# Performance work log

Hardware: AMD Instinct MI355X
Metric: run time of the kernel (lower is better)

## Reference

```python
import jax, jax.numpy as jnp
import numpy as np

ALPHA = 0.5
N_NODES = 100000
N_EDGES = 1600000
D_IN = 128
D_OUT = 128


def setup_inputs() -> dict:
    key = jax.random.key(0)
    k1, k2, k3, k4, k5, k6 = jax.random.split(key, 6)
    x = jax.random.normal(k1, (N_NODES, D_IN), dtype=jnp.float32)
    edge_index = jax.random.randint(k2, (2, N_EDGES), 0, N_NODES, dtype=jnp.int64)
    # torch Linear default init: U(-1/sqrt(fan_in), 1/sqrt(fan_in)); scale similar here
    s = 1.0 / np.sqrt(D_IN)
    W_src = jax.random.uniform(k3, (D_OUT, D_IN), jnp.float32, -s, s)
    b_src = jax.random.uniform(k4, (D_OUT,), jnp.float32, -s, s)
    W_dst = jax.random.uniform(k5, (D_OUT, D_IN), jnp.float32, -s, s)
    b_dst = jax.random.uniform(k6, (D_OUT,), jnp.float32, -s, s)
    return {"x": x, "edge_index": edge_index, "W_src": W_src, "b_src": b_src,
            "W_dst": W_dst, "b_dst": b_dst}


def _inv_sqrt(deg):
    # deg^{-1/2} with inf -> 0 (isolated nodes)
    return jnp.where(deg > 0, jax.lax.rsqrt(jnp.maximum(deg, 1e-30)), 0.0)


def reference(x, edge_index, W_src, b_src, W_dst, b_dst):
    n = x.shape[0]
    row, col = edge_index[0], edge_index[1]
    ones = jnp.ones(row.shape[0], dtype=x.dtype)
    # degrees of directed adjacency A[row, col] = 1
    deg_out = jax.ops.segment_sum(ones, row, num_segments=n)  # row sums
    deg_in = jax.ops.segment_sum(ones, col, num_segments=n)   # col sums
    # D_out^{-1/2} A D_in^{-1/2} edge weights; transpose norm yields the SAME weights
    w = _inv_sqrt(deg_out)[row] * _inv_sqrt(deg_in)[col]      # [E]
    # adj_norm @ x : aggregate sources (col) into destinations (row)
    agg_fwd = jax.ops.segment_sum(w[:, None] * x[col], row, num_segments=n)  # [N, D_IN]
    # adj_t_norm @ x : aggregate destinations (row) into sources (col)
    agg_bwd = jax.ops.segment_sum(w[:, None] * x[row], col, num_segments=n)  # [N, D_IN]
    out = ALPHA * (agg_fwd @ W_src.T + b_src) + (1.0 - ALPHA) * (agg_bwd @ W_dst.T + b_dst)
    return out
```

## Files before the change

kernel.cpp:

```cpp
#include <hip/hip_runtime.h>
#include <stdint.h>

#define D 128
#define CC 4096
#define CE 2048

typedef __attribute__((ext_vector_type(8))) __bf16 bf16x8;
typedef __attribute__((ext_vector_type(4))) float floatx4;

union FragU { uint4 u; bf16x8 b; };

__device__ __forceinline__ float bf16_lo(uint32_t u) { return __uint_as_float(u << 16); }
__device__ __forceinline__ float bf16_hi(uint32_t u) { return __uint_as_float(u & 0xffff0000u); }
__device__ __forceinline__ uint16_t f32_to_bf16(float f) {
    uint32_t u = __float_as_uint(f);
    uint32_t r = u + 0x7fffu + ((u >> 16) & 1u);
    return (uint16_t)(r >> 16);
}
__device__ __forceinline__ uint32_t pack2(float a, float b) {
    return (uint32_t)f32_to_bf16(a) | ((uint32_t)f32_to_bf16(b) << 16);
}

__global__ __launch_bounds__(256) void k_prep_w(
    const float* __restrict__ Wsrc, const float* __restrict__ bsrc,
    const float* __restrict__ Wdst, const float* __restrict__ bdst,
    uint16_t* __restrict__ WcatT, float* __restrict__ bias)
{
    int t = blockIdx.x * 256 + threadIdx.x;
    if (t < 16384) {
        WcatT[t] = f32_to_bf16(0.5f * Wsrc[t]);
        if (t < 128) bias[t] = 0.5f * (bsrc[t] + bdst[t]);
    } else {
        WcatT[t] = f32_to_bf16(0.5f * Wdst[t - 16384]);
    }
}

__global__ __launch_bounds__(256) void k_count(
    const int* __restrict__ ei, int E, int nbuk, uint32_t* __restrict__ gcount)
{
    __shared__ uint32_t cnt[1024];
    int nb2 = 2 * nbuk;
    for (int j = threadIdx.x; j < nb2; j += 256) cnt[j] = 0;
    __syncthreads();
    int base = blockIdx.x * CC;
    int lim = min(CC, E - base);
    for (int i = threadIdx.x; i < lim; i += 256) {
        int r = ei[base + i];
        int c = ei[E + base + i];
        atomicAdd(&cnt[r >> 8], 1u);
        atomicAdd(&cnt[nbuk + (c >> 8)], 1u);
    }
    __syncthreads();
    for (int j = threadIdx.x; j < nb2; j += 256) {
        uint32_t v = cnt[j];
        if (v) atomicAdd(&gcount[j], v);
    }
}

__global__ __launch_bounds__(256) void k_bases(
    const uint32_t* __restrict__ gcount, uint32_t* __restrict__ pbase,
    uint32_t* __restrict__ gcursor, int nb2)
{
    __shared__ uint32_t s[256];
    uint32_t v[4]; uint32_t tsum = 0;
    int b0 = threadIdx.x * 4;
    #pragma unroll
    for (int j = 0; j < 4; ++j) { v[j] = (b0 + j < nb2) ? gcount[b0 + j] : 0u; tsum += v[j]; }
    s[threadIdx.x] = tsum;
    __syncthreads();
    for (int off = 1; off < 256; off <<= 1) {
        uint32_t t = (threadIdx.x >= (unsigned)off) ? s[threadIdx.x - off] : 0u;
        __syncthreads();
        s[threadIdx.x] += t;
        __syncthreads();
    }
    uint32_t run = s[threadIdx.x] - tsum;
    #pragma unroll
    for (int j = 0; j < 4; ++j) {
        if (b0 + j < nb2) { pbase[b0 + j] = run; gcursor[b0 + j] = run; }
        run += v[j];
    }
}

__global__ __launch_bounds__(256) void k_part(
    const int* __restrict__ ei, int E, int nbuk,
    uint32_t* __restrict__ gcursor, uint32_t* __restrict__ gpairs)
{
    __shared__ uint32_t cnt[1024];
    __shared__ uint32_t loff[1024];
    __shared__ uint32_t gbase[1024];
    __shared__ uint32_t spair[2 * CE];
    __shared__ uint16_t sbid[2 * CE];
    __shared__ uint32_t ssum[256];
    int nb2 = 2 * nbuk;
    for (int j = threadIdx.x; j < nb2; j += 256) cnt[j] = 0;
    __syncthreads();
    int base = blockIdx.x * CE;
    int lim = min(CE, E - base);
    for (int i = threadIdx.x; i < lim; i += 256) {
        int r = ei[base + i];
        int c = ei[E + base + i];
        atomicAdd(&cnt[r >> 8], 1u);
        atomicAdd(&cnt[nbuk + (c >> 8)], 1u);
    }
    __syncthreads();
    uint32_t v0 = 0, v1 = 0, v2 = 0, v3 = 0;
    int b0 = threadIdx.x * 4;
    if (b0 < nb2)     v0 = cnt[b0];
    if (b0 + 1 < nb2) v1 = cnt[b0 + 1];
    if (b0 + 2 < nb2) v2 = cnt[b0 + 2];
    if (b0 + 3 < nb2) v3 = cnt[b0 + 3];
    uint32_t tsum = v0 + v1 + v2 + v3;
    ssum[threadIdx.x] = tsum;
    __syncthreads();
    for (int off = 1; off < 256; off <<= 1) {
        uint32_t t = (threadIdx.x >= (unsigned)off) ? ssum[threadIdx.x - off] : 0u;
        __syncthreads();
        ssum[threadIdx.x] += t;
        __syncthreads();
    }
    uint32_t run = ssum[threadIdx.x] - tsum;
    if (b0 < nb2)     loff[b0]     = run;
    if (b0 + 1 < nb2) loff[b0 + 1] = run + v0;
    if (b0 + 2 < nb2) loff[b0 + 2] = run + v0 + v1;
    if (b0 + 3 < nb2) loff[b0 + 3] = run + v0 + v1 + v2;
    __syncthreads();
    for (int j = threadIdx.x; j < nb2; j += 256) {
        uint32_t c2 = cnt[j];
        gbase[j] = c2 ? atomicAdd(&gcursor[j], c2) : 0u;
        cnt[j] = loff[j];
    }
    __syncthreads();
    for (int i = threadIdx.x; i < lim; i += 256) {
        int r = ei[base + i];
        int c = ei[E + base + i];
        int bf = r >> 8;
        uint32_t sf = atomicAdd(&cnt[bf], 1u);
        spair[sf] = ((uint32_t)c << 8) | (uint32_t)(r & 255);
        sbid[sf] = (uint16_t)bf;
        int bb = nbuk + (c >> 8);
        uint32_t sb = atomicAdd(&cnt[bb], 1u);
        spair[sb] = ((uint32_t)r << 8) | (uint32_t)(c & 255);
        sbid[sb] = (uint16_t)bb;
    }
    __syncthreads();
    int total = 2 * lim;
    for (int s2 = threadIdx.x; s2 < total; s2 += 256) {
        int b = sbid[s2];
        gpairs[gbase[b] + ((uint32_t)s2 - loff[b])] = spair[s2];
    }
}

__global__ __launch_bounds__(256) void k_build(
    const uint32_t* __restrict__ gpairs, const uint32_t* __restrict__ pbase,
    const uint32_t* __restrict__ gcount, int nbuk, int N,
    int* __restrict__ edata, uint32_t* __restrict__ ptrg, uint32_t* __restrict__ degg,
    float* __restrict__ inv_o, float* __restrict__ inv_i)
{
    __shared__ uint32_t hist[256], cur[256], ssum[256];
    int b = blockIdx.x;
    int dir = (b >= nbuk) ? 1 : 0;
    int node0 = (b - dir * nbuk) << 8;
    uint32_t base = pbase[b];
    uint32_t cnt_b = gcount[b];
    hist[threadIdx.x] = 0;
    __syncthreads();
    for (uint32_t i = threadIdx.x; i < cnt_b; i += 256)
        atomicAdd(&hist[gpairs[base + i] & 255u], 1u);
    __syncthreads();
    uint32_t h = hist[threadIdx.x];
    ssum[threadIdx.x] = h;
    __syncthreads();
    for (int off = 1; off < 256; off <<= 1) {
        uint32_t t = (threadIdx.x >= (unsigned)off) ? ssum[threadIdx.x - off] : 0u;
        __syncthreads();
        ssum[threadIdx.x] += t;
        __syncthreads();
    }
    uint32_t excl = ssum[threadIdx.x] - h;
    cur[threadIdx.x] = excl;
    int n = node0 + threadIdx.x;
    if (n < N) {
        ptrg[dir * N + n] = base + excl;
        degg[dir * N + n] = h;
        float iv = h ? rsqrtf((float)h) : 0.0f;
        if (dir == 0) inv_o[n] = iv; else inv_i[n] = iv;
    }
    __syncthreads();
    for (uint32_t i = threadIdx.x; i < cnt_b; i += 256) {
        uint32_t e = gpairs[base + i];
        uint32_t pos = atomicAdd(&cur[e & 255u], 1u);
        edata[base + pos] = (int)(e >> 8);
    }
}

__global__ __launch_bounds__(256, 2) void k_mm(
    const float* __restrict__ x, const uint4* __restrict__ Wt4,
    const float* __restrict__ inv_o, const float* __restrict__ inv_i,
    uint16_t* __restrict__ u2b, uint16_t* __restrict__ v2b, int N)
{
    const int lane = threadIdx.x & 63;
    const int m16 = lane & 15;
    const int quad = lane >> 4;
    const int mat = blockIdx.x & 1;
    uint16_t* outb = mat ? v2b : u2b;
    const float* inv = mat ? inv_o : inv_i;

    bf16x8 Bf[8][4];
    #pragma unroll
    for (int ct = 0; ct < 8; ++ct) {
        #pragma unroll
        for (int ks = 0; ks < 4; ++ks) {
            int n = mat * 128 + ct * 16 + m16;
            FragU f; f.u = Wt4[n * 16 + ks * 4 + quad];
            Bf[ct][ks] = f.b;
        }
    }

    const int ntiles = (N + 15) >> 4;
    const int wslot = (blockIdx.x >> 1) * 4 + (threadIdx.x >> 6);
    const int nslot = (gridDim.x >> 1) * 4;

    for (int t = wslot; t < ntiles; t += nslot) {
        int rowA = t * 16 + m16;
        if (rowA >= N) rowA = N - 1;
        const float4* xr = (const float4*)(x + (long)rowA * 128);
        bf16x8 Af[4];
        #pragma unroll
        for (int ks = 0; ks < 4; ++ks) {
            float4 p0 = xr[ks * 8 + quad * 2];
            float4 p1 = xr[ks * 8 + quad * 2 + 1];
            FragU f;
            f.u.x = pack2(p0.x, p0.y);
            f.u.y = pack2(p0.z, p0.w);
            f.u.z = pack2(p1.x, p1.y);
            f.u.w = pack2(p1.z, p1.w);
            Af[ks] = f.b;
        }
        float iv[4];
        #pragma unroll
        for (int r = 0; r < 4; ++r) {
            int row = t * 16 + quad * 4 + r;
            iv[r] = inv[row < N ? row : 0];
        }
        #pragma unroll
        for (int ct = 0; ct < 8; ++ct) {
            floatx4 acc = {};
            #pragma unroll
            for (int ks = 0; ks < 4; ++ks)
                acc = __builtin_amdgcn_mfma_f32_16x16x32_bf16(Af[ks], Bf[ct][ks], acc, 0, 0, 0);
            #pragma unroll
            for (int r = 0; r < 4; ++r) {
                int row = t * 16 + quad * 4 + r;
                if (row < N)
                    outb[(long)row * 128 + ct * 16 + m16] = f32_to_bf16(acc[r] * iv[r]);
            }
        }
    }
}

__global__ __launch_bounds__(256) void k_gather(
    const uint32_t* __restrict__ u2, const uint32_t* __restrict__ v2,
    const int* __restrict__ edata,
    const uint32_t* __restrict__ ptrg, const uint32_t* __restrict__ degg,
    const float* __restrict__ inv_out, const float* __restrict__ inv_in,
    const float2* __restrict__ bias2, float2* __restrict__ out2, int N)
{
    int lane = threadIdx.x & 63;
    int node = blockIdx.x * 4 + (threadIdx.x >> 6);
    if (node >= N) return;

    uint32_t s0 = ptrg[node],     d0 = degg[node];
    uint32_t s1 = ptrg[N + node], d1 = degg[N + node];

    float fx = 0, fy = 0, bx = 0, by = 0;
    uint32_t k = 0;
    for (; k + 4 <= d0; k += 4) {
        int c0 = edata[s0 + k], c1 = edata[s0 + k + 1];
        int c2 = edata[s0 + k + 2], c3 = edata[s0 + k + 3];
        uint32_t p0 = u2[(long)c0 * 64 + lane];
        uint32_t p1 = u2[(long)c1 * 64 + lane];
        uint32_t p2 = u2[(long)c2 * 64 + lane];
        uint32_t p3 = u2[(long)c3 * 64 + lane];
        fx += bf16_lo(p0) + bf16_lo(p1) + bf16_lo(p2) + bf16_lo(p3);
        fy += bf16_hi(p0) + bf16_hi(p1) + bf16_hi(p2) + bf16_hi(p3);
    }
    for (; k < d0; ++k) {
        uint32_t p = u2[(long)edata[s0 + k] * 64 + lane];
        fx += bf16_lo(p); fy += bf16_hi(p);
    }
    k = 0;
    for (; k + 4 <= d1; k += 4) {
        int c0 = edata[s1 + k], c1 = edata[s1 + k + 1];
        int c2 = edata[s1 + k + 2], c3 = edata[s1 + k + 3];
        uint32_t p0 = v2[(long)c0 * 64 + lane];
        uint32_t p1 = v2[(long)c1 * 64 + lane];
        uint32_t p2 = v2[(long)c2 * 64 + lane];
        uint32_t p3 = v2[(long)c3 * 64 + lane];
        bx += bf16_lo(p0) + bf16_lo(p1) + bf16_lo(p2) + bf16_lo(p3);
        by += bf16_hi(p0) + bf16_hi(p1) + bf16_hi(p2) + bf16_hi(p3);
    }
    for (; k < d1; ++k) {
        uint32_t p = v2[(long)edata[s1 + k] * 64 + lane];
        bx += bf16_lo(p); by += bf16_hi(p);
    }

    float io = inv_out[node], ii = inv_in[node];
    float2 b = bias2[lane];
    out2[(long)node * 64 + lane] =
        make_float2(io * fx + ii * bx + b.x, io * fy + ii * by + b.y);
}

extern "C" void kernel_launch(void* const* d_in, const int* in_sizes, int n_in,
                              void* d_out, int out_size, void* d_ws, size_t ws_size,
                              hipStream_t stream) {
    const int N = in_sizes[0] / D;
    const int E = in_sizes[1] / 2;
    const int nbuk = (N + 255) >> 8;
    const int nb2 = 2 * nbuk;

    const float* x    = (const float*)d_in[0];
    const int*   ei   = (const int*)d_in[1];
    const float* Wsrc = (const float*)d_in[2];
    const float* bsrc = (const float*)d_in[3];
    const float* Wdst = (const float*)d_in[4];
    const float* bdst = (const float*)d_in[5];

    char* ws = (char*)d_ws;
    size_t off = 0;
    uint32_t* gcount = (uint32_t*)(ws + off); off += 1024 * 4;
    uint32_t* pbase  = (uint32_t*)(ws + off); off += 1024 * 4;
    uint32_t* gcur   = (uint32_t*)(ws + off); off += 1024 * 4;
    float*    inv_o  = (float*)(ws + off);    off += (size_t)N * 4;
    float*    inv_i  = (float*)(ws + off);    off += (size_t)N * 4;
    float*    biasc  = (float*)(ws + off);    off += 128 * 4;
    uint16_t* WcatT  = (uint16_t*)(ws + off); off += (size_t)256 * 128 * 2;
    uint32_t* ptrg   = (uint32_t*)(ws + off); off += (size_t)2 * N * 4;
    uint32_t* degg   = (uint32_t*)(ws + off); off += (size_t)2 * N * 4;
    uint32_t* gpairs = (uint32_t*)(ws + off); off += (size_t)2 * E * 4;
    int*      edata  = (int*)(ws + off);      off += (size_t)2 * E * 4;
    uint32_t* u2     = (uint32_t*)(ws + off); off += (size_t)N * 64 * 4;
    uint32_t* v2     = (uint32_t*)(ws + off); off += (size_t)N * 64 * 4;

    hipMemsetAsync(gcount, 0, 1024 * 4, stream);

    k_prep_w<<<128, 256, 0, stream>>>(Wsrc, bsrc, Wdst, bdst, WcatT, biasc);
    k_count<<<(E + CC - 1) / CC, 256, 0, stream>>>(ei, E, nbuk, gcount);
    k_bases<<<1, 256, 0, stream>>>(gcount, pbase, gcur, nb2);
    k_part<<<(E + CE - 1) / CE, 256, 0, stream>>>(ei, E, nbuk, gcur, gpairs);
    k_build<<<nb2, 256, 0, stream>>>(gpairs, pbase, gcount, nbuk, N,
                                     edata, ptrg, degg, inv_o, inv_i);

    k_mm<<<1024, 256, 0, stream>>>(x, (const uint4*)WcatT, inv_o, inv_i,
                                   (uint16_t*)u2, (uint16_t*)v2, N);

    k_gather<<<(N + 3) / 4, 256, 0, stream>>>(u2, v2, edata, ptrg, degg,
                                              inv_o, inv_i, (const float2*)biasc,
                                              (float2*)d_out, N);
}
```

Measured before the change: 358.9 us.

## Fold weight prep into matmul, enlarge edge chunks, unroll gather by eight

Removes the separate weight-conversion kernel: k_mm now reads the fp32 weights directly and converts them to bf16 with the 0.5 scale, and the gather kernel computes the combined bias inline. Chunk sizes for the count and partition kernels are doubled, which means fewer blocks. The gather inner loops are unrolled to eight outstanding loads instead of four. Together these cut one launch and raise memory-level parallelism, at the cost of redundant weight conversion in every matmul block and more register pressure in the gather.

Measured after the change: 365.5 us. About the same (+1.8%).

```diff
diff --git a/kernel.cpp b/kernel.cpp
--- a/kernel.cpp
+++ b/kernel.cpp
@@ -2,8 +2,8 @@
 #include <stdint.h>
 
 #define D 128
-#define CC 4096
-#define CE 2048
+#define CC 8192
+#define CE 4096
 
 typedef __attribute__((ext_vector_type(8))) __bf16 bf16x8;
 typedef __attribute__((ext_vector_type(4))) float floatx4;
@@ -19,20 +19,6 @@
 }
 __device__ __forceinline__ uint32_t pack2(float a, float b) {
     return (uint32_t)f32_to_bf16(a) | ((uint32_t)f32_to_bf16(b) << 16);
-}
-
-__global__ __launch_bounds__(256) void k_prep_w(
-    const float* __restrict__ Wsrc, const float* __restrict__ bsrc,
-    const float* __restrict__ Wdst, const float* __restrict__ bdst,
-    uint16_t* __restrict__ WcatT, float* __restrict__ bias)
-{
-    int t = blockIdx.x * 256 + threadIdx.x;
-    if (t < 16384) {
-        WcatT[t] = f32_to_bf16(0.5f * Wsrc[t]);
-        if (t < 128) bias[t] = 0.5f * (bsrc[t] + bdst[t]);
-    } else {
-        WcatT[t] = f32_to_bf16(0.5f * Wdst[t - 16384]);
-    }
 }
 
 __global__ __launch_bounds__(256) void k_count(
@@ -195,7 +181,8 @@
 }
 
 __global__ __launch_bounds__(256, 2) void k_mm(
-    const float* __restrict__ x, const uint4* __restrict__ Wt4,
+    const float* __restrict__ x,
+    const float* __restrict__ Wsrc, const float* __restrict__ Wdst,
     const float* __restrict__ inv_o, const float* __restrict__ inv_i,
     uint16_t* __restrict__ u2b, uint16_t* __restrict__ v2b, int N)
 {
@@ -205,14 +192,20 @@
     const int mat = blockIdx.x & 1;
     uint16_t* outb = mat ? v2b : u2b;
     const float* inv = mat ? inv_o : inv_i;
+    const float* Wm = mat ? Wdst : Wsrc;
 
     bf16x8 Bf[8][4];
     #pragma unroll
     for (int ct = 0; ct < 8; ++ct) {
         #pragma unroll
         for (int ks = 0; ks < 4; ++ks) {
-            int n = mat * 128 + ct * 16 + m16;
-            FragU f; f.u = Wt4[n * 16 + ks * 4 + quad];
+            const float4* wr = (const float4*)(Wm + (ct * 16 + m16) * 128 + ks * 32 + quad * 8);
+            float4 w0 = wr[0], w1 = wr[1];
+            FragU f;
+            f.u.x = pack2(0.5f * w0.x, 0.5f * w0.y);
+            f.u.y = pack2(0.5f * w0.z, 0.5f * w0.w);
+            f.u.z = pack2(0.5f * w1.x, 0.5f * w1.y);
+            f.u.w = pack2(0.5f * w1.z, 0.5f * w1.w);
             Bf[ct][ks] = f.b;
         }
     }
@@ -264,7 +257,8 @@
     const int* __restrict__ edata,
     const uint32_t* __restrict__ ptrg, const uint32_t* __restrict__ degg,
     const float* __restrict__ inv_out, const float* __restrict__ inv_in,
-    const float2* __restrict__ bias2, float2* __restrict__ out2, int N)
+    const float* __restrict__ bsrc, const float* __restrict__ bdst,
+    float2* __restrict__ out2, int N)
 {
     int lane = threadIdx.x & 63;
     int node = blockIdx.x * 4 + (threadIdx.x >> 6);
@@ -275,30 +269,38 @@
 
     float fx = 0, fy = 0, bx = 0, by = 0;
     uint32_t k = 0;
-    for (; k + 4 <= d0; k += 4) {
-        int c0 = edata[s0 + k], c1 = edata[s0 + k + 1];
-        int c2 = edata[s0 + k + 2], c3 = edata[s0 + k + 3];
-        uint32_t p0 = u2[(long)c0 * 64 + lane];
-        uint32_t p1 = u2[(long)c1 * 64 + lane];
-        uint32_t p2 = u2[(long)c2 * 64 + lane];
-        uint32_t p3 = u2[(long)c3 * 64 + lane];
-        fx += bf16_lo(p0) + bf16_lo(p1) + bf16_lo(p2) + bf16_lo(p3);
-        fy += bf16_hi(p0) + bf16_hi(p1) + bf16_hi(p2) + bf16_hi(p3);
+    for (; k + 8 <= d0; k += 8) {
+        uint32_t p0 = u2[(long)edata[s0 + k]     * 64 + lane];
+        uint32_t p1 = u2[(long)edata[s0 + k + 1] * 64 + lane];
+        uint32_t p2 = u2[(long)edata[s0 + k + 2] * 64 + lane];
+        uint32_t p3 = u2[(long)edata[s0 + k + 3] * 64 + lane];
+        uint32_t p4 = u2[(long)edata[s0 + k + 4] * 64 + lane];
+        uint32_t p5 = u2[(long)edata[s0 + k + 5] * 64 + lane];
+        uint32_t p6 = u2[(long)edata[s0 + k + 6] * 64 + lane];
+        uint32_t p7 = u2[(long)edata[s0 + k + 7] * 64 + lane];
+        fx += bf16_lo(p0) + bf16_lo(p1) + bf16_lo(p2) + bf16_lo(p3)
+            + bf16_lo(p4) + bf16_lo(p5) + bf16_lo(p6) + bf16_lo(p7);
+        fy += bf16_hi(p0) + bf16_hi(p1) + bf16_hi(p2) + bf16_hi(p3)
+            + bf16_hi(p4) + bf16_hi(p5) + bf16_hi(p6) + bf16_hi(p7);
     }
     for (; k < d0; ++k) {
         uint32_t p = u2[(long)edata[s0 + k] * 64 + lane];
         fx += bf16_lo(p); fy += bf16_hi(p);
     }
     k = 0;
-    for (; k + 4 <= d1; k += 4) {
-        int c0 = edata[s1 + k], c1 = edata[s1 + k + 1];
-        int c2 = edata[s1 + k + 2], c3 = edata[s1 + k + 3];
-        uint32_t p0 = v2[(long)c0 * 64 + lane];
-        uint32_t p1 = v2[(long)c1 * 64 + lane];
-        uint32_t p2 = v2[(long)c2 * 64 + lane];
-        uint32_t p3 = v2[(long)c3 * 64 + lane];
-        bx += bf16_lo(p0) + bf16_lo(p1) + bf16_lo(p2) + bf16_lo(p3);
-        by += bf16_hi(p0) + bf16_hi(p1) + bf16_hi(p2) + bf16_hi(p3);
+    for (; k + 8 <= d1; k += 8) {
+        uint32_t p0 = v2[(long)edata[s1 + k]     * 64 + lane];
+        uint32_t p1 = v2[(long)edata[s1 + k + 1] * 64 + lane];
+        uint32_t p2 = v2[(long)edata[s1 + k + 2] * 64 + lane];
+        uint32_t p3 = v2[(long)edata[s1 + k + 3] * 64 + lane];
+        uint32_t p4 = v2[(long)edata[s1 + k + 4] * 64 + lane];
+        uint32_t p5 = v2[(long)edata[s1 + k + 5] * 64 + lane];
+        uint32_t p6 = v2[(long)edata[s1 + k + 6] * 64 + lane];
+        uint32_t p7 = v2[(long)edata[s1 + k + 7] * 64 + lane];
+        bx += bf16_lo(p0) + bf16_lo(p1) + bf16_lo(p2) + bf16_lo(p3)
+            + bf16_lo(p4) + bf16_lo(p5) + bf16_lo(p6) + bf16_lo(p7);
+        by += bf16_hi(p0) + bf16_hi(p1) + bf16_hi(p2) + bf16_hi(p3)
+            + bf16_hi(p4) + bf16_hi(p5) + bf16_hi(p6) + bf16_hi(p7);
     }
     for (; k < d1; ++k) {
         uint32_t p = v2[(long)edata[s1 + k] * 64 + lane];
@@ -306,9 +308,10 @@
     }
 
     float io = inv_out[node], ii = inv_in[node];
-    float2 b = bias2[lane];
+    float b0 = 0.5f * (bsrc[2 * lane]     + bdst[2 * lane]);
+    float b1 = 0.5f * (bsrc[2 * lane + 1] + bdst[2 * lane + 1]);
     out2[(long)node * 64 + lane] =
-        make_float2(io * fx + ii * bx + b.x, io * fy + ii * by + b.y);
+        make_float2(io * fx + ii * bx + b0, io * fy + ii * by + b1);
 }
 
 extern "C" void kernel_launch(void* const* d_in, const int* in_sizes, int n_in,
@@ -333,8 +336,6 @@
     uint32_t* gcur   = (uint32_t*)(ws + off); off += 1024 * 4;
     float*    inv_o  = (float*)(ws + off);    off += (size_t)N * 4;
     float*    inv_i  = (float*)(ws + off);    off += (size_t)N * 4;
-    float*    biasc  = (float*)(ws + off);    off += 128 * 4;
-    uint16_t* WcatT  = (uint16_t*)(ws + off); off += (size_t)256 * 128 * 2;
     uint32_t* ptrg   = (uint32_t*)(ws + off); off += (size_t)2 * N * 4;
     uint32_t* degg   = (uint32_t*)(ws + off); off += (size_t)2 * N * 4;
     uint32_t* gpairs = (uint32_t*)(ws + off); off += (size_t)2 * E * 4;
@@ -344,17 +345,16 @@
 
     hipMemsetAsync(gcount, 0, 1024 * 4, stream);
 
-    k_prep_w<<<128, 256, 0, stream>>>(Wsrc, bsrc, Wdst, bdst, WcatT, biasc);
     k_count<<<(E + CC - 1) / CC, 256, 0, stream>>>(ei, E, nbuk, gcount);
     k_bases<<<1, 256, 0, stream>>>(gcount, pbase, gcur, nb2);
     k_part<<<(E + CE - 1) / CE, 256, 0, stream>>>(ei, E, nbuk, gcur, gpairs);
     k_build<<<nb2, 256, 0, stream>>>(gpairs, pbase, gcount, nbuk, N,
                                      edata, ptrg, degg, inv_o, inv_i);
 
-    k_mm<<<1024, 256, 0, stream>>>(x, (const uint4*)WcatT, inv_o, inv_i,
+    k_mm<<<1024, 256, 0, stream>>>(x, Wsrc, Wdst, inv_o, inv_i,
                                    (uint16_t*)u2, (uint16_t*)v2, N);
 
     k_gather<<<(N + 3) / 4, 256, 0, stream>>>(u2, v2, edata, ptrg, degg,
-                                              inv_o, inv_i, (const float2*)biasc,
+                                              inv_o, inv_i, bsrc, bdst,
                                               (float2*)d_out, N);
 }
```
